# Kernel tuning notes

Measured on AMD Instinct MI355X. Metric: run time of the kernel, lower is better.

Reference implementation:

```python
import jax, jax.numpy as jnp
import numpy as np

T, B, H, W_IMG = 8, 4, 128, 128
NUM_CLS = 21
LEAK = 0.99   # config.leak_mem
THR = 1.0     # config.def_threshold
EPS = 1e-4    # BatchNorm2d eps


@jax.custom_vjp
def spike(mem):
    # Heaviside spike with 'Linear' surrogate gradient
    return (mem > THR).astype(mem.dtype)

def _spike_fwd(mem):
    return spike(mem), mem

def _spike_bwd(mem, g):
    # triangular (linear) surrogate around threshold
    return (g * jnp.maximum(0.0, 1.0 - jnp.abs(mem - THR)),)

spike.defvjp(_spike_fwd, _spike_bwd)


def conv(x, w, pad, dil=1):
    return jax.lax.conv_general_dilated(
        x, w, window_strides=(1, 1), padding=[(pad, pad), (pad, pad)],
        rhs_dilation=(dil, dil), dimension_numbers=('NCHW', 'OIHW', 'NCHW'))


def bn_apply(x, bn_t):
    # bn_t: [3, C] = (gamma, running_mean, running_var); bias=None in the model
    g, mu, var = bn_t[0], bn_t[1], bn_t[2]
    inv = (g / jnp.sqrt(var + EPS))[None, :, None, None]
    return (x - mu[None, :, None, None]) * inv


def avgpool(x):
    # AvgPool2d(kernel=3, stride=2, padding=1), count_include_pad=True -> /9
    s = jax.lax.reduce_window(x, 0.0, jax.lax.add, (1, 1, 3, 3), (1, 1, 2, 2),
                              [(0, 0), (0, 0), (1, 1), (1, 1)])
    return s / 9.0


def lif(x, w, bn_t, mem, pad, dil=1):
    # mem = leak*mem + BN_t(conv(x)); spike; soft reset by threshold
    out = bn_apply(conv(x, w, pad, dil), bn_t)
    mem = LEAK * mem + out
    s = spike(mem)
    return mem - THR * s, s


def _forward(x, u, W0, W1, W2, W3, W4, W5, W6, W7, W8,
             bn0, bn1, bn2, bn3, bn4, bn5, bn6, bn7):
    # Poisson generator: spike when u <= |x|, carrying sign of x. [T,B,3,H,W]
    spk_in = jnp.where(u <= jnp.abs(x)[None], jnp.sign(x)[None], 0.0)
    z = lambda c, h: jnp.zeros((B, c, h, h), x.dtype)
    init = (z(64, 128), z(64, 128), z(128, 64), z(128, 64),
            z(256, 32), z(256, 32), z(256, 32), z(1024, 32), z(NUM_CLS, 32))

    def step(carry, xs):
        m0, m1, m2, m3, m4, m5, m6, m7, macc = carry
        sp, b0, b1, b2, b3, b4, b5, b6, b7 = xs
        m0, o = lif(sp, W0, b0, m0, 1)
        m1, o = lif(o, W1, b1, m1, 1)
        o = avgpool(o)                      # 128 -> 64
        m2, o = lif(o, W2, b2, m2, 1)
        m3, o = lif(o, W3, b3, m3, 1)
        o = avgpool(o)                      # 64 -> 32
        m4, o = lif(o, W4, b4, m4, 1)
        m5, o = lif(o, W5, b5, m5, 2, 2)    # atrous256
        m6, o = lif(o, W6, b6, m6, 2, 2)    # atrous256
        m7, o = lif(o, W7, b7, m7, 12, 12)  # classifier atrous1024
        macc = macc + conv(o, W8, 0)        # output layer accumulates voltage
        return (m0, m1, m2, m3, m4, m5, m6, m7, macc), None

    carry, _ = jax.lax.scan(step, init, (spk_in, bn0, bn1, bn2, bn3, bn4, bn5, bn6, bn7))
    return carry[-1] / T


def setup_inputs() -> dict:
    key = jax.random.key(0)
    ks = jax.random.split(key, 24)

    def w(k, shape):
        fan_in = int(np.prod(shape[1:]))
        return jax.random.normal(k, shape, jnp.float32) / np.sqrt(fan_in)

    def bn(k, c):
        return jax.random.uniform(k, (T, 3, c), jnp.float32, 0.25, 1.25)

    inp = {
        'x': jax.random.normal(ks[0], (B, 3, H, W_IMG), jnp.float32),
        'u': jax.random.uniform(ks[1], (T, B, 3, H, W_IMG), jnp.float32),
        'W0': w(ks[2], (64, 3, 3, 3)),
        'W1': w(ks[3], (64, 64, 3, 3)),
        'W2': w(ks[4], (128, 64, 3, 3)),
        'W3': w(ks[5], (128, 128, 3, 3)),
        'W4': w(ks[6], (256, 128, 3, 3)),
        'W5': w(ks[7], (256, 256, 3, 3)),
        'W6': w(ks[8], (256, 256, 3, 3)),
        'W7': w(ks[9], (1024, 256, 3, 3)),
        'W8': w(ks[10], (NUM_CLS, 1024, 1, 1)),
        'bn0': bn(ks[11], 64), 'bn1': bn(ks[12], 64),
        'bn2': bn(ks[13], 128), 'bn3': bn(ks[14], 128),
        'bn4': bn(ks[15], 256), 'bn5': bn(ks[16], 256),
        'bn6': bn(ks[17], 256), 'bn7': bn(ks[18], 1024),
    }
    return inp


def reference(x, u, W0, W1, W2, W3, W4, W5, W6, W7, W8,
              bn0, bn1, bn2, bn3, bn4, bn5, bn6, bn7):
    return _forward(x, u, W0, W1, W2, W3, W4, W5, W6, W7, W8,
                    bn0, bn1, bn2, bn3, bn4, bn5, bn6, bn7)
```

## Files before the change

kernel.cpp:

```cpp
#include <hip/hip_runtime.h>
#include <hip/hip_bf16.h>
#include <cstddef>
#include <cstdint>

#define LEAK  0.99f
#define THRS  1.0f
#define BNEPS 1e-4f

static constexpr int TT   = 8;
static constexpr int BB   = 4;
static constexpr int NCLS = 21;

typedef __attribute__((ext_vector_type(8))) short short8v;
typedef __attribute__((ext_vector_type(4))) float f32x4;

__global__ void zero_f32(float* __restrict__ p, int n) {
  int i = blockIdx.x * blockDim.x + threadIdx.x;
  int stride = gridDim.x * blockDim.x;
  for (; i < n; i += stride) p[i] = 0.0f;
}

__global__ void scale_f32(float* __restrict__ p, int n, float s) {
  int i = blockIdx.x * blockDim.x + threadIdx.x;
  if (i < n) p[i] *= s;
}

__global__ void wsplit(const float* __restrict__ Wsrc,
                       __hip_bfloat16* __restrict__ whi, __hip_bfloat16* __restrict__ wlo,
                       int Co, int Ci, int Cip, float scale) {
  const int Kpad = 9 * Cip;
  const int n = Co * Kpad;
  int i = blockIdx.x * 256 + threadIdx.x;
  if (i >= n) return;
  int co = i / Kpad, k = i - co * Kpad;
  int tap = k / Cip, ci = k - tap * Cip;
  float w = 0.0f;
  if (ci < Ci) w = Wsrc[((size_t)co * Ci + ci) * 9 + tap] * scale;
  __hip_bfloat16 h = __float2bfloat16(w);
  float r = w - __bfloat162float(h);
  whi[i] = h;
  wlo[i] = __float2bfloat16(r);
}

__global__ void spike_gen(const float* __restrict__ x, const float* __restrict__ u,
                          __hip_bfloat16* __restrict__ spk) {
  const int HW = 128 * 128;
  int i = blockIdx.x * 256 + threadIdx.x;
  if (i >= BB * HW) return;
  int b = i / HW, hw = i - b * HW;
#pragma unroll
  for (int c = 0; c < 3; ++c) {
    float xv = x[((size_t)b * 3 + c) * HW + hw];
    float uv = u[((size_t)b * 3 + c) * HW + hw];
    float ax = fabsf(xv);
    float sg = (xv > 0.0f) ? 1.0f : ((xv < 0.0f) ? -1.0f : 0.0f);
    float s  = (uv <= ax) ? sg : 0.0f;
    spk[(size_t)i * 32 + c] = __float2bfloat16(s);
  }
}

template<int M, int N, int GRP, int CPT>
__global__ __launch_bounds__(256) void gemm_lif(
    const __hip_bfloat16* __restrict__ actin,
    const __hip_bfloat16* __restrict__ wsp,
    const float* __restrict__ bnt,
    float* __restrict__ mem, __hip_bfloat16* __restrict__ actout,
    const __hip_bfloat16* __restrict__ zp,
    int Co, int lgHW, int lgW, int dil, int lgGX) {
  constexpr int NW = 4;
  constexpr int Cip = CPT * 32;
  constexpr int Kpad = 9 * Cip;
  constexpr int lgcpt = (CPT == 1) ? 0 : (CPT == 2) ? 1 : (CPT == 4) ? 2 : 3;
  constexpr int R  = N * 32;
  constexpr int lgR = (N == 1) ? 5 : ((N == 2) ? 6 : 7);
  constexpr int BUFROWS = GRP * R;
  constexpr int BUFELEM = BUFROWS * 32;
  constexpr int INSTS = BUFROWS / (16 * NW);
  constexpr int AM = M * GRP;
  constexpr int WAITN = INSTS + AM;
  constexpr int NGRP = (9 * CPT) / GRP;
  static_assert((9 * CPT) % GRP == 0, "group must divide chunk count");
  __shared__ __hip_bfloat16 lds[3 * BUFELEM];

  const int HW = 1 << lgHW, H = HW >> lgW, W = 1 << lgW;
  const unsigned CoKpad = (unsigned)Co * Kpad;
  const int lane = threadIdx.x & 63, wid = threadIdx.x >> 6;
  const int l15 = lane & 15, g = lane >> 4;

  const int nb = gridDim.x;
  const int flat = blockIdx.x;
  const int swz = (flat & 7) * (nb >> 3) + (flat >> 3);
  const int bx = swz & ((1 << lgGX) - 1);
  const int by = swz >> lgGX;
  const int p0  = (bx * NW + wid) * (M * 16);
  const int co0 = by * (N * 16);

  int b_[M], y_[M], x_[M];
#pragma unroll
  for (int m = 0; m < M; ++m) {
    int pb = p0 + m * 16;
    b_[m] = pb >> lgHW;
    int rem = pb & (HW - 1);
    y_[m] = rem >> lgW;
    x_[m] = (rem & (W - 1)) + l15;
  }

  unsigned sgb[INSTS];
#pragma unroll
  for (int i = 0; i < INSTS; ++i) {
    int f  = wid * (BUFROWS / NW) + i * 16 + (lane >> 2);
    int cc = f >> lgR;
    int r  = f & (R - 1);
    int half = r >> (lgR - 1);
    int co   = r & (16 * N - 1);
    int slot = (lane & 3) ^ ((co >> 1) & 3);
    sgb[i] = (unsigned)half * CoKpad + (unsigned)(co0 + co) * Kpad + slot * 8 + cc * 32;
  }

  auto stage = [&](int grp, int buf) {
#pragma unroll
    for (int i = 0; i < INSTS; ++i) {
      const __hip_bfloat16* gp = wsp + sgb[i] + grp * (GRP * 32);
      __hip_bfloat16* lp = &lds[buf * BUFELEM + (wid * (BUFROWS / NW) + i * 16) * 32];
      __builtin_amdgcn_global_load_lds(
          (const __attribute__((address_space(1))) void*)gp,
          (__attribute__((address_space(3))) void*)lp, 16, 0, 0);
    }
  };

  const __hip_bfloat16* apc[M];
  auto mkaddr = [&](int tap) {
    int ty = (tap * 11) >> 5;
    int tx = tap - ty * 3;
    int dy = (ty - 1) * dil, dx = (tx - 1) * dil;
#pragma unroll
    for (int m = 0; m < M; ++m) {
      int sy = y_[m] + dy, sx = x_[m] + dx;
      bool v = (sy >= 0) & (sy < H) & (sx >= 0) & (sx < W);
      int pix = (b_[m] << lgHW) + (sy << lgW) + sx;
      apc[m] = v ? (actin + (size_t)pix * Cip + 8 * g) : (zp + 8 * g);
    }
  };

  auto prefA = [&](int grp, short8v (&dst)[GRP][M]) {
#pragma unroll
    for (int cc = 0; cc < GRP; ++cc) {
      int c = grp * GRP + cc;
      if ((c & (CPT - 1)) == 0) mkaddr(c >> lgcpt);
      int kc = (c & (CPT - 1)) << 5;
#pragma unroll
      for (int m = 0; m < M; ++m)
        dst[cc][m] = *(const short8v*)(apc[m] + kc);
    }
  };

  f32x4 acc[M][N] = {};
  const int rdb = l15 * 32 + ((g ^ ((l15 >> 1) & 3)) * 8);

  short8v aA[GRP][M], aB[GRP][M];

  auto grp_body = [&](int gi, int bc, short8v (&aU)[GRP][M], short8v (&aF)[GRP][M]) {
    asm volatile("s_waitcnt vmcnt(%0)" :: "n"(WAITN) : "memory");
    __builtin_amdgcn_s_barrier();
    __builtin_amdgcn_sched_barrier(0);

    if (gi + 1 < NGRP) prefA(gi + 1, aF);
    __builtin_amdgcn_sched_barrier(0);
    if (gi + 2 < NGRP) {
      int b2 = bc + 2; if (b2 >= 3) b2 -= 3;
      stage(gi + 2, b2);
    }

    const __hip_bfloat16* bp = &lds[bc * BUFELEM];
#pragma unroll
    for (int cc = 0; cc < GRP; ++cc) {
      short8v bh[N], bl[N];
#pragma unroll
      for (int j = 0; j < N; ++j) {
        bh[j] = *(const short8v*)(bp + cc * (R * 32) + j * 512 + rdb);
        bl[j] = *(const short8v*)(bp + cc * (R * 32) + (N * 512) + j * 512 + rdb);
      }
      __builtin_amdgcn_s_setprio(1);
#pragma unroll
      for (int j = 0; j < N; ++j)
#pragma unroll
        for (int m = 0; m < M; ++m) {
          acc[m][j] = __builtin_amdgcn_mfma_f32_16x16x32_bf16(aU[cc][m], bh[j], acc[m][j], 0, 0, 0);
          acc[m][j] = __builtin_amdgcn_mfma_f32_16x16x32_bf16(aU[cc][m], bl[j], acc[m][j], 0, 0, 0);
        }
      __builtin_amdgcn_s_setprio(0);
    }
  };

  stage(0, 0);
  __builtin_amdgcn_sched_barrier(0);
  prefA(0, aA);
  __builtin_amdgcn_sched_barrier(0);
  if (NGRP > 1) stage(1, 1);

#pragma unroll
  for (int gi = 0; gi < NGRP; ++gi) {
    const int bc = gi % 3;
    if (gi & 1) grp_body(gi, bc, aB, aA);
    else        grp_body(gi, bc, aA, aB);
  }

#pragma unroll
  for (int j = 0; j < N; ++j) {
    int c = co0 + j * 16 + l15;
    float ga = bnt[c], mu = bnt[Co + c], va = bnt[2 * Co + c];
    float sc = ga / sqrtf(va + BNEPS);
#pragma unroll
    for (int m = 0; m < M; ++m) {
      int pixb = p0 + m * 16 + 4 * g;
#pragma unroll
      for (int r = 0; r < 4; ++r) {
        size_t idx = (size_t)(pixb + r) * Co + c;
        float bno = (acc[m][j][r] - mu) * sc;
        float mv = LEAK * mem[idx] + bno;
        float s = (mv > THRS) ? 1.0f : 0.0f;
        actout[idx] = __float2bfloat16(s);
        mem[idx] = mv - s;
      }
    }
  }
}

__global__ void avgpool_sum8(const __hip_bfloat16* __restrict__ in,
                             __hip_bfloat16* __restrict__ out, int C, int H, int W) {
  const int Ho = H >> 1, Wo = W >> 1;
  const int C8 = C >> 3;
  const int n = BB * Ho * Wo * C8;
  int i = blockIdx.x * 256 + threadIdx.x;
  if (i >= n) return;
  int c8 = i % C8; int t = i / C8;
  int xo = t % Wo; t /= Wo;
  int yo = t % Ho; int b = t / Ho;
  const int y0 = 2 * yo - 1, x0 = 2 * xo - 1;
  float s[8] = {0, 0, 0, 0, 0, 0, 0, 0};
#pragma unroll
  for (int dy = 0; dy < 3; ++dy) {
    int iy = y0 + dy;
    if (iy < 0 || iy >= H) continue;
#pragma unroll
    for (int dx = 0; dx < 3; ++dx) {
      int ix = x0 + dx;
      if (ix < 0 || ix >= W) continue;
      short8v v = *(const short8v*)(in + (((size_t)b * H + iy) * W + ix) * C + c8 * 8);
#pragma unroll
      for (int e = 0; e < 8; ++e) {
        __hip_bfloat16_raw raw; raw.x = (unsigned short)v[e];
        s[e] += __bfloat162float(__hip_bfloat16(raw));
      }
    }
  }
  short8v o;
#pragma unroll
  for (int e = 0; e < 8; ++e) {
    __hip_bfloat16_raw raw = __hip_bfloat16_raw(__float2bfloat16(s[e]));
    o[e] = (short)raw.x;
  }
  *(short8v*)(out + (size_t)i * 8) = o;
}

__global__ void out_conv(const __hip_bfloat16* __restrict__ act,
                         const float* __restrict__ W8, float* __restrict__ out) {
  int gw = (blockIdx.x * 256 + threadIdx.x) >> 6;
  int lane = threadIdx.x & 63;
  int b = gw >> 10, pix = gw & 1023;
  const __hip_bfloat16* ap = act + ((size_t)gw << 10);
  float acc[NCLS];
#pragma unroll
  for (int c = 0; c < NCLS; ++c) acc[c] = 0.0f;
  for (int j = 0; j < 16; ++j) {
    int ci = j * 64 + lane;
    float av = __bfloat162float(ap[ci]);
#pragma unroll
    for (int c = 0; c < NCLS; ++c) acc[c] = fmaf(av, W8[c * 1024 + ci], acc[c]);
  }
#pragma unroll
  for (int c = 0; c < NCLS; ++c) {
    float v = acc[c];
    for (int off = 32; off; off >>= 1) v += __shfl_xor(v, off, 64);
    if (lane == 0) out[((size_t)b * NCLS + c) * 1024 + pix] += v;
  }
}

extern "C" void kernel_launch(void* const* d_in, const int* in_sizes, int n_in,
                              void* d_out, int out_size, void* d_ws, size_t ws_size,
                              hipStream_t stream) {
  const float* x = (const float*)d_in[0];
  const float* u = (const float*)d_in[1];
  const float* Wc[9];
  for (int i = 0; i < 9; ++i) Wc[i] = (const float*)d_in[2 + i];
  const float* bn[8];
  for (int i = 0; i < 8; ++i) bn[i] = (const float*)d_in[11 + i];

  const int Ci_[8]  = {3, 64, 64, 128, 128, 256, 256, 256};
  const int Cip_[8] = {32, 64, 64, 128, 128, 256, 256, 256};
  const int Co_[8]  = {64, 64, 128, 128, 256, 256, 256, 1024};
  const int HH_[8]  = {128, 128, 64, 64, 32, 32, 32, 32};
  const float wsc_[8] = {1.f, 1.f, 1.f / 9.f, 1.f, 1.f / 9.f, 1.f, 1.f, 1.f};

  float* ws = (float*)d_ws;
  size_t off = 0;
  auto align8 = [](size_t v) { return (v + 7) & ~(size_t)7; };

  float* memp[8];
  for (int i = 0; i < 8; ++i) {
    memp[i] = ws + off;
    off += (size_t)BB * HH_[i] * HH_[i] * Co_[i];
  }
  __hip_bfloat16* spk = (__hip_bfloat16*)(ws + off);
  off += (size_t)BB * 16384 * 32 / 2;
  __hip_bfloat16* zp = (__hip_bfloat16*)(ws + off);
  off += 256;
  const size_t zero_floats = off;
  __hip_bfloat16* actA = (__hip_bfloat16*)(ws + off); off += 2097152;
  __hip_bfloat16* actB = (__hip_bfloat16*)(ws + off); off += 2097152;
  __hip_bfloat16* wall[8];
  for (int i = 0; i < 8; ++i) {
    size_t n = (size_t)Co_[i] * 9 * Cip_[i];
    wall[i] = (__hip_bfloat16*)(ws + off);
    off = align8(off + n);
  }

  zero_f32<<<2048, 256, 0, stream>>>(ws, (int)zero_floats);
  zero_f32<<<(BB * NCLS * 1024 + 255) / 256, 256, 0, stream>>>((float*)d_out, BB * NCLS * 1024);

  for (int i = 0; i < 8; ++i) {
    int n = Co_[i] * 9 * Cip_[i];
    wsplit<<<(n + 255) / 256, 256, 0, stream>>>(Wc[i], wall[i], wall[i] + n,
                                                Co_[i], Ci_[i], Cip_[i], wsc_[i]);
  }

  const size_t uT = (size_t)BB * 3 * 16384;
  for (int t = 0; t < TT; ++t) {
    spike_gen<<<(BB * 16384 + 255) / 256, 256, 0, stream>>>(x, u + (size_t)t * uT, spk);
    gemm_lif<2, 4, 3, 1><<<512, 256, 0, stream>>>(spk,  wall[0], bn[0] + (size_t)t * 3 * 64,   memp[0], actA, zp, 64,   14, 7, 1, 9);
    gemm_lif<2, 4, 3, 2><<<512, 256, 0, stream>>>(actA, wall[1], bn[1] + (size_t)t * 3 * 64,   memp[1], actB, zp, 64,   14, 7, 1, 9);
    avgpool_sum8<<<(BB * 64 * 64 * 8 + 255) / 256, 256, 0, stream>>>(actB, actA, 64, 128, 128);
    gemm_lif<2, 2, 3, 2><<<512, 256, 0, stream>>>(actA, wall[2], bn[2] + (size_t)t * 3 * 128,  memp[2], actB, zp, 128,  12, 6, 1, 7);
    gemm_lif<2, 2, 4, 4><<<512, 256, 0, stream>>>(actB, wall[3], bn[3] + (size_t)t * 3 * 128,  memp[3], actA, zp, 128,  12, 6, 1, 7);
    avgpool_sum8<<<(BB * 32 * 32 * 16 + 255) / 256, 256, 0, stream>>>(actA, actB, 128, 64, 64);
    gemm_lif<1, 2, 4, 4><<<512, 256, 0, stream>>>(actB, wall[4], bn[4] + (size_t)t * 3 * 256,   memp[4], actA, zp, 256,  10, 5, 1, 6);
    gemm_lif<1, 2, 6, 8><<<512, 256, 0, stream>>>(actA, wall[5], bn[5] + (size_t)t * 3 * 256,   memp[5], actB, zp, 256,  10, 5, 2, 6);
    gemm_lif<1, 2, 6, 8><<<512, 256, 0, stream>>>(actB, wall[6], bn[6] + (size_t)t * 3 * 256,   memp[6], actA, zp, 256,  10, 5, 2, 6);
    gemm_lif<2, 4, 3, 8><<<512, 256, 0, stream>>>(actA, wall[7], bn[7] + (size_t)t * 3 * 1024, memp[7], actB, zp, 1024, 10, 5, 12, 5);
    out_conv<<<dim3(BB * 1024 / 4), 256, 0, stream>>>(actB, Wc[8], (float*)d_out);
  }
  scale_f32<<<(BB * NCLS * 1024 + 255) / 256, 256, 0, stream>>>((float*)d_out, BB * NCLS * 1024, 1.0f / TT);
}
```

Baseline: 2.058 ms.

## Add intra-block split-K across wave groups with LDS reduction and double buffering

Result: no change. 2.020 ms (-1.8%).

```diff
diff --git a/kernel.cpp b/kernel.cpp
--- a/kernel.cpp
+++ b/kernel.cpp
@@ -59,8 +59,8 @@
   }
 }
 
-template<int M, int N, int GRP, int CPT>
-__global__ __launch_bounds__(256) void gemm_lif(
+template<int M, int N, int GRP, int CPT, int SPLIT>
+__global__ __launch_bounds__(SPLIT * 256, 4) void gemm_lif(
     const __hip_bfloat16* __restrict__ actin,
     const __hip_bfloat16* __restrict__ wsp,
     const float* __restrict__ bnt,
@@ -77,22 +77,26 @@
   constexpr int BUFELEM = BUFROWS * 32;
   constexpr int INSTS = BUFROWS / (16 * NW);
   constexpr int AM = M * GRP;
-  constexpr int WAITN = INSTS + AM;
-  constexpr int NGRP = (9 * CPT) / GRP;
-  static_assert((9 * CPT) % GRP == 0, "group must divide chunk count");
-  __shared__ __hip_bfloat16 lds[3 * BUFELEM];
+  constexpr int WAITN = AM;
+  constexpr int NCH = (9 * CPT) / SPLIT;
+  constexpr int NGRP = NCH / GRP;
+  static_assert(NCH % GRP == 0, "group must divide per-half chunk count");
+  __shared__ __hip_bfloat16 lds[SPLIT * 2 * BUFELEM];
 
   const int HW = 1 << lgHW, H = HW >> lgW, W = 1 << lgW;
   const unsigned CoKpad = (unsigned)Co * Kpad;
   const int lane = threadIdx.x & 63, wid = threadIdx.x >> 6;
+  const int kw = wid >> 2;
+  const int wq = wid & 3;
   const int l15 = lane & 15, g = lane >> 4;
+  __hip_bfloat16* ldsh = lds + kw * 2 * BUFELEM;
 
   const int nb = gridDim.x;
   const int flat = blockIdx.x;
   const int swz = (flat & 7) * (nb >> 3) + (flat >> 3);
   const int bx = swz & ((1 << lgGX) - 1);
   const int by = swz >> lgGX;
-  const int p0  = (bx * NW + wid) * (M * 16);
+  const int p0  = (bx * NW + wq) * (M * 16);
   const int co0 = by * (N * 16);
 
   int b_[M], y_[M], x_[M];
@@ -105,23 +109,25 @@
     x_[m] = (rem & (W - 1)) + l15;
   }
 
+  const unsigned kbase = (unsigned)kw * (NCH * 32);
   unsigned sgb[INSTS];
 #pragma unroll
   for (int i = 0; i < INSTS; ++i) {
-    int f  = wid * (BUFROWS / NW) + i * 16 + (lane >> 2);
+    int f  = wq * (BUFROWS / NW) + i * 16 + (lane >> 2);
     int cc = f >> lgR;
     int r  = f & (R - 1);
     int half = r >> (lgR - 1);
     int co   = r & (16 * N - 1);
     int slot = (lane & 3) ^ ((co >> 1) & 3);
-    sgb[i] = (unsigned)half * CoKpad + (unsigned)(co0 + co) * Kpad + slot * 8 + cc * 32;
-  }
-
-  auto stage = [&](int grp, int buf) {
+    sgb[i] = (unsigned)half * CoKpad + (unsigned)(co0 + co) * Kpad + slot * 8
+           + cc * 32 + kbase;
+  }
+
+  auto stage = [&](int gl, int buf) {
 #pragma unroll
     for (int i = 0; i < INSTS; ++i) {
-      const __hip_bfloat16* gp = wsp + sgb[i] + grp * (GRP * 32);
-      __hip_bfloat16* lp = &lds[buf * BUFELEM + (wid * (BUFROWS / NW) + i * 16) * 32];
+      const __hip_bfloat16* gp = wsp + sgb[i] + gl * (GRP * 32);
+      __hip_bfloat16* lp = &ldsh[buf * BUFELEM + (wq * (BUFROWS / NW) + i * 16) * 32];
       __builtin_amdgcn_global_load_lds(
           (const __attribute__((address_space(1))) void*)gp,
           (__attribute__((address_space(3))) void*)lp, 16, 0, 0);
@@ -142,11 +148,11 @@
     }
   };
 
-  auto prefA = [&](int grp, short8v (&dst)[GRP][M]) {
+  auto prefA = [&](int gl, short8v (&dst)[GRP][M], bool first) {
 #pragma unroll
     for (int cc = 0; cc < GRP; ++cc) {
-      int c = grp * GRP + cc;
-      if ((c & (CPT - 1)) == 0) mkaddr(c >> lgcpt);
+      int c = kw * NCH + gl * GRP + cc;
+      if ((c & (CPT - 1)) == 0 || (first && cc == 0)) mkaddr(c >> lgcpt);
       int kc = (c & (CPT - 1)) << 5;
 #pragma unroll
       for (int m = 0; m < M; ++m)
@@ -159,19 +165,17 @@
 
   short8v aA[GRP][M], aB[GRP][M];
 
-  auto grp_body = [&](int gi, int bc, short8v (&aU)[GRP][M], short8v (&aF)[GRP][M]) {
+  auto grp_body = [&](int gi, short8v (&aU)[GRP][M], short8v (&aF)[GRP][M]) {
     asm volatile("s_waitcnt vmcnt(%0)" :: "n"(WAITN) : "memory");
     __builtin_amdgcn_s_barrier();
     __builtin_amdgcn_sched_barrier(0);
 
-    if (gi + 1 < NGRP) prefA(gi + 1, aF);
-    __builtin_amdgcn_sched_barrier(0);
-    if (gi + 2 < NGRP) {
-      int b2 = bc + 2; if (b2 >= 3) b2 -= 3;
-      stage(gi + 2, b2);
-    }
-
-    const __hip_bfloat16* bp = &lds[bc * BUFELEM];
+    if (gi + 1 < NGRP) {
+      stage(gi + 1, (gi + 1) & 1);
+      prefA(gi + 1, aF, false);
+    }
+
+    const __hip_bfloat16* bp = &ldsh[(gi & 1) * BUFELEM];
 #pragma unroll
     for (int cc = 0; cc < GRP; ++cc) {
       short8v bh[N], bl[N];
@@ -193,16 +197,37 @@
   };
 
   stage(0, 0);
-  __builtin_amdgcn_sched_barrier(0);
-  prefA(0, aA);
-  __builtin_amdgcn_sched_barrier(0);
-  if (NGRP > 1) stage(1, 1);
+  prefA(0, aA, true);
 
 #pragma unroll
   for (int gi = 0; gi < NGRP; ++gi) {
-    const int bc = gi % 3;
-    if (gi & 1) grp_body(gi, bc, aB, aA);
-    else        grp_body(gi, bc, aA, aB);
+    if (gi & 1) grp_body(gi, aB, aA);
+    else        grp_body(gi, aA, aB);
+  }
+
+  if constexpr (SPLIT == 2) {
+    asm volatile("s_waitcnt vmcnt(0) lgkmcnt(0)" ::: "memory");
+    __builtin_amdgcn_s_barrier();
+    f32x4* red = (f32x4*)lds;
+    const int rbase = (wq * 64 + lane) * (M * N);
+    if (kw == 1) {
+#pragma unroll
+      for (int m = 0; m < M; ++m)
+#pragma unroll
+        for (int j = 0; j < N; ++j)
+          red[rbase + m * N + j] = acc[m][j];
+    }
+    asm volatile("s_waitcnt lgkmcnt(0)" ::: "memory");
+    __builtin_amdgcn_s_barrier();
+    if (kw == 1) return;
+#pragma unroll
+    for (int m = 0; m < M; ++m)
+#pragma unroll
+      for (int j = 0; j < N; ++j) {
+        f32x4 t = red[rbase + m * N + j];
+#pragma unroll
+        for (int r = 0; r < 4; ++r) acc[m][j][r] += t[r];
+      }
   }
 
 #pragma unroll
@@ -337,16 +362,16 @@
   const size_t uT = (size_t)BB * 3 * 16384;
   for (int t = 0; t < TT; ++t) {
     spike_gen<<<(BB * 16384 + 255) / 256, 256, 0, stream>>>(x, u + (size_t)t * uT, spk);
-    gemm_lif<2, 4, 3, 1><<<512, 256, 0, stream>>>(spk,  wall[0], bn[0] + (size_t)t * 3 * 64,   memp[0], actA, zp, 64,   14, 7, 1, 9);
-    gemm_lif<2, 4, 3, 2><<<512, 256, 0, stream>>>(actA, wall[1], bn[1] + (size_t)t * 3 * 64,   memp[1], actB, zp, 64,   14, 7, 1, 9);
+    gemm_lif<2, 2, 3, 1, 1><<<1024, 256, 0, stream>>>(spk,  wall[0], bn[0] + (size_t)t * 3 * 64,   memp[0], actA, zp, 64,   14, 7, 1, 9);
+    gemm_lif<2, 2, 3, 2, 1><<<1024, 256, 0, stream>>>(actA, wall[1], bn[1] + (size_t)t * 3 * 64,   memp[1], actB, zp, 64,   14, 7, 1, 9);
     avgpool_sum8<<<(BB * 64 * 64 * 8 + 255) / 256, 256, 0, stream>>>(actB, actA, 64, 128, 128);
-    gemm_lif<2, 2, 3, 2><<<512, 256, 0, stream>>>(actA, wall[2], bn[2] + (size_t)t * 3 * 128,  memp[2], actB, zp, 128,  12, 6, 1, 7);
-    gemm_lif<2, 2, 4, 4><<<512, 256, 0, stream>>>(actB, wall[3], bn[3] + (size_t)t * 3 * 128,  memp[3], actA, zp, 128,  12, 6, 1, 7);
+    gemm_lif<2, 2, 3, 2, 2><<<512, 512, 0, stream>>>(actA, wall[2], bn[2] + (size_t)t * 3 * 128,  memp[2], actB, zp, 128,  12, 6, 1, 7);
+    gemm_lif<2, 2, 3, 4, 2><<<512, 512, 0, stream>>>(actB, wall[3], bn[3] + (size_t)t * 3 * 128,  memp[3], actA, zp, 128,  12, 6, 1, 7);
     avgpool_sum8<<<(BB * 32 * 32 * 16 + 255) / 256, 256, 0, stream>>>(actA, actB, 128, 64, 64);
-    gemm_lif<1, 2, 4, 4><<<512, 256, 0, stream>>>(actB, wall[4], bn[4] + (size_t)t * 3 * 256,   memp[4], actA, zp, 256,  10, 5, 1, 6);
-    gemm_lif<1, 2, 6, 8><<<512, 256, 0, stream>>>(actA, wall[5], bn[5] + (size_t)t * 3 * 256,   memp[5], actB, zp, 256,  10, 5, 2, 6);
-    gemm_lif<1, 2, 6, 8><<<512, 256, 0, stream>>>(actB, wall[6], bn[6] + (size_t)t * 3 * 256,   memp[6], actA, zp, 256,  10, 5, 2, 6);
-    gemm_lif<2, 4, 3, 8><<<512, 256, 0, stream>>>(actA, wall[7], bn[7] + (size_t)t * 3 * 1024, memp[7], actB, zp, 1024, 10, 5, 12, 5);
+    gemm_lif<1, 2, 3, 4, 2><<<512, 512, 0, stream>>>(actB, wall[4], bn[4] + (size_t)t * 3 * 256,   memp[4], actA, zp, 256,  10, 5, 1, 6);
+    gemm_lif<1, 2, 4, 8, 2><<<512, 512, 0, stream>>>(actA, wall[5], bn[5] + (size_t)t * 3 * 256,   memp[5], actB, zp, 256,  10, 5, 2, 6);
+    gemm_lif<1, 2, 4, 8, 2><<<512, 512, 0, stream>>>(actB, wall[6], bn[6] + (size_t)t * 3 * 256,   memp[6], actA, zp, 256,  10, 5, 2, 6);
+    gemm_lif<2, 4, 2, 8, 2><<<512, 512, 0, stream>>>(actA, wall[7], bn[7] + (size_t)t * 3 * 1024, memp[7], actB, zp, 1024, 10, 5, 12, 5);
     out_conv<<<dim3(BB * 1024 / 4), 256, 0, stream>>>(actB, Wc[8], (float*)d_out);
   }
   scale_f32<<<(BB * NCLS * 1024 + 255) / 256, 256, 0, stream>>>((float*)d_out, BB * NCLS * 1024, 1.0f / TT);
```
